# Kernel optimization log

Measured on AMD Instinct MI355X. Metric: run time of the kernel, lower is better.

The kernel has to match this reference:

```python
import jax, jax.numpy as jnp
import numpy as np

N_USERS = 100000
N_LOCAS = 50000
N = N_USERS + N_LOCAS
D = 128   # embedding_dynamic_size
K = 128   # kg entity dim
S = 128   # static dim
NK = 50000  # kg rows
E = 2048  # number of events
LN_EPS = 1e-5
NORM_EPS = 1e-12


def setup_inputs() -> dict:
    key = jax.random.key(0)
    ks = jax.random.split(key, 24)
    f = jnp.float32
    rin = D + K + 1
    s_rnn = 1.0 / np.sqrt(D)
    s_pred = 1.0 / np.sqrt(2 * S + 2 * D + K)
    inp = {
        'embedding': jax.random.normal(ks[0], (N, D), f),
        'static': jax.random.normal(ks[1], (N, S), f),
        'kg': jax.random.normal(ks[2], (NK, K), f),
        'W_ih_u': jax.random.normal(ks[3], (D, rin), f) * s_rnn,
        'b_ih_u': jax.random.normal(ks[4], (D,), f) * s_rnn,
        'W_hh_u': jax.random.normal(ks[5], (D, D), f) * s_rnn,
        'b_hh_u': jax.random.normal(ks[6], (D,), f) * s_rnn,
        'W_ih_l': jax.random.normal(ks[7], (D, rin), f) * s_rnn,
        'b_ih_l': jax.random.normal(ks[8], (D,), f) * s_rnn,
        'W_hh_l': jax.random.normal(ks[9], (D, D), f) * s_rnn,
        'b_hh_l': jax.random.normal(ks[10], (D,), f) * s_rnn,
        'w_proj': jax.random.normal(ks[11], (D,), f),   # NormalLinear(1, D) weight, std=1/sqrt(1)=1
        'b_proj': jax.random.normal(ks[12], (D,), f),
        'ln_g': jnp.ones((D + K,), f),
        'ln_b': jnp.zeros((D + K,), f),
        'W_pred': jax.random.normal(ks[13], (S + D, 2 * S + 2 * D + K), f) * s_pred,
        'b_pred': jnp.zeros((S + D,), f),
        'delta_u': jax.random.uniform(ks[14], (E,), f),
        'delta_l': jax.random.uniform(ks[15], (E,), f),
        'idx_user': jax.random.randint(ks[16], (E,), 0, N_USERS, jnp.int32),
        'idx_loca': jax.random.randint(ks[17], (E,), 0, N_LOCAS, jnp.int32),
        'idx_prev': jax.random.randint(ks[18], (E,), 0, N_LOCAS, jnp.int32),
        'idx_know': jax.random.randint(ks[19], (E,), 0, NK, jnp.int32),
        'num_users': N_USERS,
    }
    return inp


def reference(embedding, static, kg, W_ih_u, b_ih_u, W_hh_u, b_hh_u,
              W_ih_l, b_ih_l, W_hh_l, b_hh_l, w_proj, b_proj, ln_g, ln_b,
              W_pred, b_pred, delta_u, delta_l,
              idx_user, idx_loca, idx_prev, idx_know, num_users):
    sg = jax.lax.stop_gradient

    def l2n(x):  # F.normalize along the feature dim (row vector)
        return x / jnp.maximum(jnp.linalg.norm(x), NORM_EPS)

    # event index preprocessing (matches idx_loca + num_users etc.)
    xs = (idx_user, idx_loca + num_users, idx_prev + num_users, idx_know,
          delta_u, delta_l)

    def step(carry, ev):
        emb, loss = carry
        iu, il, ip, ik, du, dl = ev
        u = emb[iu]        # [D]
        l = emb[il]        # [D]
        p = emb[ip]        # [D]
        kgr = kg[ik]       # [K]
        # projection: u * (1 + Linear(1->D)(delta_u))
        proj = u * (1.0 + w_proj * du + b_proj)
        # layer_norm over concat([emb_prev, kg_row]) of size D+K
        x = jnp.concatenate([p, kgr])
        mu = x.mean()
        var = jnp.mean((x - mu) ** 2)
        ln = (x - mu) / jnp.sqrt(var + LN_EPS) * ln_g + ln_b
        meta = jnp.concatenate([proj, ln, static[ip], static[iu]])  # [2S+2D+K]
        pred = W_pred @ meta + b_pred                               # [S+D]
        tgt = jnp.concatenate([l, static[il]])
        loss_pred = jnp.mean((pred - sg(tgt)) ** 2)
        # RNNCell updates (tanh), then L2-normalize
        x_u = jnp.concatenate([l, kgr, du[None]])
        new_u = l2n(jnp.tanh(W_ih_u @ x_u + b_ih_u + W_hh_u @ u + b_hh_u))
        x_l = jnp.concatenate([u, kgr, dl[None]])
        new_l = l2n(jnp.tanh(W_ih_l @ x_l + b_ih_l + W_hh_l @ l + b_hh_l))
        loss = loss + loss_pred \
                    + jnp.mean((new_u - sg(u)) ** 2) \
                    + jnp.mean((new_l - sg(l)) ** 2)
        emb = emb.at[iu].set(new_u).at[il].set(new_l)
        return (emb, loss), None

    (emb, loss), _ = jax.lax.scan(
        step, (embedding, jnp.asarray(0.0, embedding.dtype)), xs)
    return emb, loss
```

## Files before the change

### kernel.cpp

```cpp
#include <hip/hip_runtime.h>

#define DEVINL static __device__ __forceinline__

typedef float f32x4 __attribute__((ext_vector_type(4)));

constexpr int NUSER = 100000;
constexpr int D     = 128;
constexpr int METAN = 640;
constexpr int NT    = 256;
constexpr int CH    = 4;
constexpr int KP4   = 160;
constexpr int KR4   = 96;
constexpr int NCPY  = 1024;
constexpr int STW   = 640;

struct Params {
  const float *emb_in, *stat, *kg;
  const float *Wihu, *bihu, *Whhu, *bhhu;
  const float *Wihl, *bihl, *Whhl, *bhhl;
  const float *wproj, *bproj, *lng, *lnb, *Wpred, *bpred;
  const float *deltau, *deltal;
  const int *idxu, *idxl, *idxp, *idxk;
  float *emb;
  float *loss_slot;
  float *WpredT;
  float *WrnnT;
  float *brnn;
  float *wcol;
  float *loss_ev;
  float *stash;
  int *cnt_u, *cnt_w, *cnt_t;
  int *flag_u, *flag_l;
  int *done;
  int E, N, NLOC, NWORK;
};

DEVINL float loadx(const float* p) {
  return __hip_atomic_load(p, __ATOMIC_RELAXED, __HIP_MEMORY_SCOPE_AGENT);
}
DEVINL void storex(float* p, float v) {
  __hip_atomic_store(p, v, __ATOMIC_RELAXED, __HIP_MEMORY_SCOPE_AGENT);
}
DEVINL int loadcnt(const int* p) {
  return __hip_atomic_load(p, __ATOMIC_RELAXED, __HIP_MEMORY_SCOPE_AGENT);
}
DEVINL void storei(int* p, int v) {
  __hip_atomic_store(p, v, __ATOMIC_RELAXED, __HIP_MEMORY_SCOPE_AGENT);
}
DEVINL void sigadd(int* pp) {
  __hip_atomic_fetch_add(pp, 1, __ATOMIC_RELAXED, __HIP_MEMORY_SCOPE_AGENT);
}
DEVINL float dot4(float4 a, float4 b) { return a.x*b.x + a.y*b.y + a.z*b.z + a.w*b.w; }

DEVINL float4 block_sum4(float4 v, float4* s4) {
  #pragma unroll
  for (int o = 32; o; o >>= 1) {
    v.x += __shfl_xor(v.x, o, 64); v.y += __shfl_xor(v.y, o, 64);
    v.z += __shfl_xor(v.z, o, 64); v.w += __shfl_xor(v.w, o, 64);
  }
  if ((threadIdx.x & 63) == 0) s4[threadIdx.x >> 6] = v;
  __syncthreads();
  float4 r;
  r.x = s4[0].x + s4[1].x + s4[2].x + s4[3].x;
  r.y = s4[0].y + s4[1].y + s4[2].y + s4[3].y;
  r.z = s4[0].z + s4[1].z + s4[2].z + s4[3].z;
  r.w = s4[0].w + s4[1].w + s4[2].w + s4[3].w;
  __syncthreads();
  return r;
}

DEVINL void half_sum4(float4 v, float4* s4, float4* lo, float4* hi) {
  #pragma unroll
  for (int o = 32; o; o >>= 1) {
    v.x += __shfl_xor(v.x, o, 64); v.y += __shfl_xor(v.y, o, 64);
    v.z += __shfl_xor(v.z, o, 64); v.w += __shfl_xor(v.w, o, 64);
  }
  if ((threadIdx.x & 63) == 0) s4[threadIdx.x >> 6] = v;
  __syncthreads();
  lo->x = s4[0].x + s4[1].x; lo->y = s4[0].y + s4[1].y;
  lo->z = s4[0].z + s4[1].z; lo->w = s4[0].w + s4[1].w;
  hi->x = s4[2].x + s4[3].x; hi->y = s4[2].y + s4[3].y;
  hi->z = s4[2].z + s4[3].z; hi->w = s4[2].w + s4[3].w;
  __syncthreads();
}

__global__ void k_init(Params p) {
  int tid = blockIdx.x * NT + threadIdx.x;
  int stride = gridDim.x * NT;
  for (int e = tid; e < p.E; e += stride) {
    p.flag_u[p.idxu[e]] = 1;
    p.flag_l[p.idxl[e]] = 1;
  }
  for (int idx = tid; idx < 256 * KP4; idx += stride) {
    int j = idx / KP4, k4 = idx - j * KP4;
    float4 v = *(const float4*)(p.Wpred + (size_t)j * METAN + k4 * 4);
    ((float4*)p.WpredT)[k4 * 256 + j] = v;
  }
  for (int idx = tid; idx < 256 * KR4; idx += stride) {
    int j = idx / KR4, k4 = idx - j * KR4;
    int i = j & 127;
    const float* Wih = (j < 128) ? p.Wihu : p.Wihl;
    const float* Whh = (j < 128) ? p.Whhu : p.Whhl;
    float4 v; float* vp = (float*)&v;
    #pragma unroll
    for (int e = 0; e < 4; ++e) {
      int k = k4 * 4 + e;
      vp[e] = (k < 256) ? Wih[(size_t)i * 257 + k] : Whh[(size_t)i * 128 + (k - 256)];
    }
    ((float4*)p.WrnnT)[k4 * 256 + j] = v;
  }
  for (int j = tid; j < 256; j += stride) {
    int i = j & 127;
    p.brnn[j] = (j < 128) ? p.bihu[i] + p.bhhu[i] : p.bihl[i] + p.bhhl[i];
    p.wcol[j] = (j < 128) ? p.Wihu[(size_t)i * 257 + 256] : p.Wihl[(size_t)i * 257 + 256];
  }
}

__global__ __launch_bounds__(NT, 2) void k_main(Params p) {
  __shared__ __align__(16) float s_meta[CH][METAN];
  __shared__ __align__(16) float s_u[CH][D], s_l[CH][D], s_p[CH][D], s_kg[CH][D], s_sil[CH][D];
  __shared__ float4 s_r4[4];
  __shared__ unsigned long long s_redu[4][CH];
  __shared__ int s_ev[8][CH];
  __shared__ float s_dd[2][CH];

  const int tid = threadIdx.x, w = tid >> 6, lane = tid & 63;
  const int bid = blockIdx.x;

  if (bid >= p.NWORK && bid < p.NWORK + NCPY) {
    size_t gid = (size_t)(bid - p.NWORK) * NT + tid;
    size_t gs  = (size_t)NCPY * NT;
    size_t n4  = (size_t)p.N * 32;
    const f32x4* src = (const f32x4*)p.emb_in;
    f32x4* dst = (f32x4*)p.emb;
    size_t g = gid;
    for (; g + 3 * gs < n4; g += 4 * gs) {
      size_t g0 = g, g1 = g + gs, g2 = g + 2 * gs, g3 = g + 3 * gs;
      int r0 = (int)(g0 >> 5), r1 = (int)(g1 >> 5), r2 = (int)(g2 >> 5), r3 = (int)(g3 >> 5);
      int f0 = (r0 < NUSER) ? p.flag_u[r0] : p.flag_l[r0 - NUSER];
      int f1 = (r1 < NUSER) ? p.flag_u[r1] : p.flag_l[r1 - NUSER];
      int f2 = (r2 < NUSER) ? p.flag_u[r2] : p.flag_l[r2 - NUSER];
      int f3 = (r3 < NUSER) ? p.flag_u[r3] : p.flag_l[r3 - NUSER];
      f32x4 v0 = src[g0], v1 = src[g1], v2 = src[g2], v3 = src[g3];
      if (!f0) dst[g0] = v0;
      if (!f1) dst[g1] = v1;
      if (!f2) dst[g2] = v2;
      if (!f3) dst[g3] = v3;
    }
    for (; g < n4; g += gs) {
      int r = (int)(g >> 5);
      int f = (r < NUSER) ? p.flag_u[r] : p.flag_l[r - NUSER];
      f32x4 v = src[g];
      if (!f) dst[g] = v;
    }
    return;
  }

  const bool is_chain = (bid < p.NWORK);
  const int c = is_chain ? bid : bid - p.NWORK - NCPY;
  const int base = c * CH;
  const int nev = min(CH, p.E - base);
  if (nev <= 0) return;

  int iu_[CH], il_[CH], ip_[CH], ik_[CH];
  #pragma unroll
  for (int e = 0; e < CH; ++e) {
    int t = base + e; bool v = e < nev;
    iu_[e] = v ? p.idxu[t] : -1;
    il_[e] = v ? p.idxl[t] : -1;
    ip_[e] = v ? p.idxp[t] : -1;
    ik_[e] = v ? p.idxk[t] : 0;
  }

  if (is_chain) {
    float du_[CH], dl_[CH];
    #pragma unroll
    for (int e = 0; e < CH; ++e) {
      int t = base + e; bool v = e < nev;
      du_[e] = v ? p.deltau[t] : 0.f;
      dl_[e] = v ? p.deltal[t] : 0.f;
    }

    unsigned long long pk[CH] = {0ull,0ull,0ull,0ull};
    for (int s = tid; s < base; s += NT) {
      int ius = p.idxu[s], ils = p.idxl[s], ips = p.idxp[s];
      #pragma unroll
      for (int e = 0; e < CH; ++e) {
        unsigned long long a  = (ius == iu_[e]);
        unsigned long long wl = (ils == il_[e]);
        unsigned long long b  = (unsigned long long)((ils == il_[e]) + (ips == il_[e]));
        unsigned long long cc = (ils == ip_[e]);
        pk[e] += a | (wl << 16) | (b << 32) | (cc << 48);
      }
    }
    #pragma unroll
    for (int o = 32; o; o >>= 1) {
      #pragma unroll
      for (int e = 0; e < CH; ++e) pk[e] += __shfl_xor(pk[e], o, 64);
    }
    if (lane == 0) {
      #pragma unroll
      for (int e = 0; e < CH; ++e) s_redu[w][e] = pk[e];
    }
    __syncthreads();
    #pragma unroll
    for (int e = 0; e < CH; ++e)
      pk[e] = s_redu[0][e] + s_redu[1][e] + s_redu[2][e] + s_redu[3][e];
    __syncthreads();

    int A_[CH], WL_[CH], B_[CH], C_[CH];
    #pragma unroll
    for (int e = 0; e < CH; ++e) {
      int a  = (int)(pk[e] & 0xffff),        wl = (int)((pk[e] >> 16) & 0xffff);
      int b  = (int)((pk[e] >> 32) & 0xffff), cc = (int)((pk[e] >> 48) & 0xffff);
      #pragma unroll
      for (int s2 = 0; s2 < CH; ++s2) if (s2 < e) {
        a  += (iu_[s2] == iu_[e]);
        wl += (il_[s2] == il_[e]);
        b  += (il_[s2] == il_[e]) + (ip_[s2] == il_[e]);
        cc += (il_[s2] == ip_[e]);
      }
      A_[e] = a; WL_[e] = wl; B_[e] = b; C_[e] = cc;
    }
    bool internal = false;
    #pragma unroll
    for (int t2 = 1; t2 < CH; ++t2) if (t2 < nev) {
      #pragma unroll
      for (int s2 = 0; s2 < t2; ++s2)
        internal |= (iu_[s2] == iu_[t2]) | (il_[s2] == il_[t2]) |
                    (il_[s2] == ip_[t2]) | (ip_[s2] == il_[t2]);
    }

    if (tid == 0) {
      #pragma unroll
      for (int e = 0; e < CH; ++e) {
        s_ev[0][e] = iu_[e]; s_ev[1][e] = il_[e]; s_ev[2][e] = ip_[e];
        s_ev[3][e] = A_[e];  s_ev[4][e] = WL_[e]; s_ev[5][e] = B_[e];
        s_ev[6][e] = C_[e];  s_ev[7][e] = ik_[e];
        s_dd[0][e] = du_[e]; s_dd[1][e] = dl_[e];
      }
    }
    __syncthreads();

    auto PRELOAD = [&](int b0, int b1) {
      int e = w;
      if (e >= b0 && e < b1) {
        int iu = s_ev[0][e], ilr = s_ev[1][e] + NUSER, ipr = s_ev[2][e] + NUSER;
        int A = s_ev[3][e], WL = s_ev[4][e], Ck = s_ev[6][e], ik = s_ev[7][e];
        if (lane < 32) {
          int li = lane * 4;
          *(float4*)&s_kg[e][li] = *(const float4*)(p.kg + (size_t)ik * D + li);
        }
        int i0 = lane * 2;
        if (!A)  *(float2*)&s_u[e][i0] = *(const float2*)(p.emb_in + (size_t)iu  * D + i0);
        if (!WL) *(float2*)&s_l[e][i0] = *(const float2*)(p.emb_in + (size_t)ilr * D + i0);
        if (!Ck) *(float2*)&s_p[e][i0] = *(const float2*)(p.emb_in + (size_t)ipr * D + i0);
      }
    };

    auto SPIN = [&](int b0, int b1) {
      if (w == 0) {
        int e = b0 + lane;
        bool act = lane < (b1 - b0);
        int iu = 0, il = 0, ip = 0, A = 0, Bc = 0, Cc = 0;
        if (act) {
          iu = s_ev[0][e]; il = s_ev[1][e]; ip = s_ev[2][e];
          A = s_ev[3][e]; Bc = s_ev[5][e]; Cc = s_ev[6][e];
        }
        int guard = 0;
        while (true) {
          int x = loadcnt(&p.cnt_u[iu]);
          int y = loadcnt(&p.cnt_t[il]);
          int z = loadcnt(&p.cnt_w[ip]);
          bool ok = (!act) | ((x >= A) & (y >= Bc) & (z >= Cc));
          if (__all(ok)) break;
          if (++guard > (1 << 22)) break;
          __builtin_amdgcn_s_sleep(1);
        }
      }
      __syncthreads();
    };

    auto POSTLOAD = [&](int b0, int b1) {
      int e = w;
      if (e >= b0 && e < b1) {
        int iu = s_ev[0][e], ilr = s_ev[1][e] + NUSER, ipr = s_ev[2][e] + NUSER;
        int A = s_ev[3][e], WL = s_ev[4][e], Ck = s_ev[6][e];
        int i0 = lane * 2;
        if (A) {
          s_u[e][i0]   = loadx(p.emb + (size_t)iu * D + i0);
          s_u[e][i0+1] = loadx(p.emb + (size_t)iu * D + i0 + 1);
        }
        if (WL) {
          s_l[e][i0]   = loadx(p.emb + (size_t)ilr * D + i0);
          s_l[e][i0+1] = loadx(p.emb + (size_t)ilr * D + i0 + 1);
        }
        if (Ck) {
          s_p[e][i0]   = loadx(p.emb + (size_t)ipr * D + i0);
          s_p[e][i0+1] = loadx(p.emb + (size_t)ipr * D + i0 + 1);
        }
      }
    };

    auto RNNPROC = [&](int b0, int b1) {
      __syncthreads();
      const bool uc = (tid < 128);
      const float4* xo0 = (const float4*)(uc ? s_l[0] : s_u[0]);
      const float4* xo1 = (const float4*)(uc ? s_l[1] : s_u[1]);
      const float4* xo2 = (const float4*)(uc ? s_l[2] : s_u[2]);
      const float4* xo3 = (const float4*)(uc ? s_l[3] : s_u[3]);
      const float4* xk0 = (const float4*)s_kg[0];
      const float4* xk1 = (const float4*)s_kg[1];
      const float4* xk2 = (const float4*)s_kg[2];
      const float4* xk3 = (const float4*)s_kg[3];
      const float4* xs0 = (const float4*)(uc ? s_u[0] : s_l[0]);
      const float4* xs1 = (const float4*)(uc ? s_u[1] : s_l[1]);
      const float4* xs2 = (const float4*)(uc ? s_u[2] : s_l[2]);
      const float4* xs3 = (const float4*)(uc ? s_u[3] : s_l[3]);
      float ra0 = 0.f, ra1 = 0.f, ra2 = 0.f, ra3 = 0.f;
      const float4* wr = (const float4*)p.WrnnT + tid;
      #pragma unroll 8
      for (int k4 = 0; k4 < 32; ++k4) {
        float4 wv = wr[k4 * 256];
        ra0 += dot4(wv, xo0[k4]); ra1 += dot4(wv, xo1[k4]);
        ra2 += dot4(wv, xo2[k4]); ra3 += dot4(wv, xo3[k4]);
      }
      #pragma unroll 8
      for (int k4 = 32; k4 < 64; ++k4) {
        float4 wv = wr[k4 * 256];
        ra0 += dot4(wv, xk0[k4-32]); ra1 += dot4(wv, xk1[k4-32]);
        ra2 += dot4(wv, xk2[k4-32]); ra3 += dot4(wv, xk3[k4-32]);
      }
      #pragma unroll 8
      for (int k4 = 64; k4 < 96; ++k4) {
        float4 wv = wr[k4 * 256];
        ra0 += dot4(wv, xs0[k4-64]); ra1 += dot4(wv, xs1[k4-64]);
        ra2 += dot4(wv, xs2[k4-64]); ra3 += dot4(wv, xs3[k4-64]);
      }
      float brn = p.brnn[tid], wcv = p.wcol[tid];
      float d0 = uc ? s_dd[0][0] : s_dd[1][0];
      float d1 = uc ? s_dd[0][1] : s_dd[1][1];
      float d2 = uc ? s_dd[0][2] : s_dd[1][2];
      float d3 = uc ? s_dd[0][3] : s_dd[1][3];
      float h0 = tanhf(ra0 + brn + wcv * d0), h1 = tanhf(ra1 + brn + wcv * d1);
      float h2v = tanhf(ra2 + brn + wcv * d2), h3 = tanhf(ra3 + brn + wcv * d3);

      float4 SU, SL;
      half_sum4(make_float4(h0*h0, h1*h1, h2v*h2v, h3*h3), s_r4, &SU, &SL);
      float s0 = uc ? SU.x : SL.x, s1 = uc ? SU.y : SL.y;
      float s2 = uc ? SU.z : SL.z, s3 = uc ? SU.w : SL.w;
      float n0 = h0 / fmaxf(sqrtf(s0), 1e-12f), n1 = h1 / fmaxf(sqrtf(s1), 1e-12f);
      float n2 = h2v / fmaxf(sqrtf(s2), 1e-12f), n3 = h3 / fmaxf(sqrtf(s3), 1e-12f);

      float nv[CH] = {n0, n1, n2, n3};
      #pragma unroll
      for (int e = 0; e < CH; ++e) if (e >= b0 && e < b1) {
        if (tid < 128) storex(p.emb + (size_t)s_ev[0][e] * D + tid, nv[e]);
        else           storex(p.emb + ((size_t)s_ev[1][e] + NUSER) * D + (tid - 128), nv[e]);
      }
      __syncthreads();

      if (tid >= b0 && tid < b1) {
        __builtin_amdgcn_fence(__ATOMIC_RELEASE, "agent");
        sigadd(&p.cnt_u[s_ev[0][tid]]);
        sigadd(&p.cnt_t[s_ev[1][tid]]);
        sigadd(&p.cnt_w[s_ev[1][tid]]);
        sigadd(&p.cnt_t[s_ev[2][tid]]);
      }

      #pragma unroll
      for (int e = 0; e < CH; ++e) if (e >= b0 && e < b1) {
        float* st = p.stash + (size_t)(base + e) * STW;
        if (tid < 128) {
          storex(st + tid,       s_u[e][tid]);
          storex(st + 256 + tid, s_p[e][tid]);
          storex(st + 384 + tid, nv[e]);
        } else {
          int i = tid - 128;
          storex(st + 128 + i, s_l[e][i]);
          storex(st + 512 + i, nv[e]);
        }
      }
    };

    if (!internal) {
      PRELOAD(0, nev);
      SPIN(0, nev);
      POSTLOAD(0, nev);
      RNNPROC(0, nev);
    } else {
      for (int e = 0; e < nev; ++e) {
        PRELOAD(e, e + 1);
        SPIN(e, e + 1);
        POSTLOAD(e, e + 1);
        RNNPROC(e, e + 1);
      }
    }
    __syncthreads();
    if (tid == 0) storei(&p.done[c], 1);
    return;
  }

  {
    if (w == 0) {
      int guard = 0;
      while (!loadcnt(&p.done[c])) {
        if (++guard > (1 << 22)) break;
        __builtin_amdgcn_s_sleep(1);
      }
    }
    __syncthreads();

    if (w < nev) {
      int e = w;
      const float* st = p.stash + (size_t)(base + e) * STW;
      int iu = iu_[e], ilr = il_[e] + NUSER, ipr = ip_[e] + NUSER, ik = ik_[e];
      int i0 = lane * 2;
      s_u[e][i0]   = loadx(st + i0);
      s_u[e][i0+1] = loadx(st + i0 + 1);
      s_l[e][i0]   = loadx(st + 128 + i0);
      s_l[e][i0+1] = loadx(st + 128 + i0 + 1);
      s_p[e][i0]   = loadx(st + 256 + i0);
      s_p[e][i0+1] = loadx(st + 256 + i0 + 1);
      int h2 = lane >> 5, li = (lane & 31) * 4;
      if (h2 == 0) {
        *(float4*)&s_kg[e][li]         = *(const float4*)(p.kg   + (size_t)ik  * D + li);
        *(float4*)&s_meta[e][512 + li] = *(const float4*)(p.stat + (size_t)iu  * D + li);
      } else {
        *(float4*)&s_meta[e][384 + li] = *(const float4*)(p.stat + (size_t)ipr * D + li);
        *(float4*)&s_sil[e][li]        = *(const float4*)(p.stat + (size_t)ilr * D + li);
      }
    }
    __syncthreads();

    if (w < nev) {
      int e = w;
      float du = p.deltau[base + e];
      float4 xv = (lane < 32) ? *(const float4*)&s_p[e][lane * 4]
                              : *(const float4*)&s_kg[e][(lane - 32) * 4];
      float sm = xv.x + xv.y + xv.z + xv.w;
      #pragma unroll
      for (int o = 32; o; o >>= 1) sm += __shfl_xor(sm, o, 64);
      float mu = sm * (1.f / 256.f);
      float4 d = make_float4(xv.x - mu, xv.y - mu, xv.z - mu, xv.w - mu);
      float vs = d.x*d.x + d.y*d.y + d.z*d.z + d.w*d.w;
      #pragma unroll
      for (int o = 32; o; o >>= 1) vs += __shfl_xor(vs, o, 64);
      float rstd = rsqrtf(vs * (1.f / 256.f) + 1e-5f);
      int idx2 = lane * 4;
      float4 g  = *(const float4*)&p.lng[idx2];
      float4 bb = *(const float4*)&p.lnb[idx2];
      float4 lnv = make_float4(d.x*rstd*g.x + bb.x, d.y*rstd*g.y + bb.y,
                               d.z*rstd*g.z + bb.z, d.w*rstd*g.w + bb.w);
      if (lane < 32) *(float4*)&s_meta[e][128 + idx2] = lnv;
      else           *(float4*)&s_meta[e][128 + idx2] = lnv;
      int i0 = lane * 2;
      #pragma unroll
      for (int j = 0; j < 2; ++j) {
        int i = i0 + j;
        s_meta[e][i] = s_u[e][i] * (1.f + p.wproj[i] * du + p.bproj[i]);
      }
    }
    __syncthreads();

    const bool uc = (tid < 128);
    const float4* m40 = (const float4*)&s_meta[0][0];
    const float4* m41 = (const float4*)&s_meta[1][0];
    const float4* m42 = (const float4*)&s_meta[2][0];
    const float4* m43 = (const float4*)&s_meta[3][0];
    float pa0 = 0.f, pa1 = 0.f, pa2 = 0.f, pa3 = 0.f;
    const float4* wp = (const float4*)p.WpredT + tid;
    #pragma unroll 8
    for (int k4 = 0; k4 < KP4; ++k4) {
      float4 wv = wp[k4 * 256];
      pa0 += dot4(wv, m40[k4]); pa1 += dot4(wv, m41[k4]);
      pa2 += dot4(wv, m42[k4]); pa3 += dot4(wv, m43[k4]);
    }
    float bp = p.bpred[tid];
    float4 ep2;
    {
      float tg0 = uc ? s_l[0][tid] : s_sil[0][tid - 128];
      float tg1 = uc ? s_l[1][tid] : s_sil[1][tid - 128];
      float tg2 = uc ? s_l[2][tid] : s_sil[2][tid - 128];
      float tg3 = uc ? s_l[3][tid] : s_sil[3][tid - 128];
      float e0 = pa0 + bp - tg0, e1 = pa1 + bp - tg1;
      float e2 = pa2 + bp - tg2, e3 = pa3 + bp - tg3;
      ep2 = make_float4(e0*e0, e1*e1, e2*e2, e3*e3);
    }
    float4 LP = block_sum4(ep2, s_r4);

    const float* st0 = p.stash + (size_t)(base + 0) * STW;
    const float* st1 = p.stash + (size_t)(base + 1) * STW;
    const float* st2 = p.stash + (size_t)(base + 2) * STW;
    const float* st3 = p.stash + (size_t)(base + 3) * STW;
    int noff = uc ? (384 + tid) : (512 + tid - 128);
    float n0 = loadx(st0 + noff), n1 = loadx(st1 + noff);
    float n2 = loadx(st2 + noff), n3 = loadx(st3 + noff);
    float o0 = uc ? s_u[0][tid] : s_l[0][tid - 128];
    float o1 = uc ? s_u[1][tid] : s_l[1][tid - 128];
    float o2 = uc ? s_u[2][tid] : s_l[2][tid - 128];
    float o3 = uc ? s_u[3][tid] : s_l[3][tid - 128];
    float q0 = n0 - o0, q1 = n1 - o1, q2 = n2 - o2, q3 = n3 - o3;
    float4 LE = block_sum4(make_float4(q0*q0, q1*q1, q2*q2, q3*q3), s_r4);

    if (tid < nev) {
      float lp = (tid == 0) ? LP.x : (tid == 1) ? LP.y : (tid == 2) ? LP.z : LP.w;
      float le = (tid == 0) ? LE.x : (tid == 1) ? LE.y : (tid == 2) ? LE.z : LE.w;
      p.loss_ev[base + tid] = lp * (1.f / 256.f) + le * (1.f / 128.f);
    }
  }
}

__global__ void k_fin(Params p) {
  __shared__ float4 s_r4[4];
  float v = 0.f;
  for (int i = threadIdx.x; i < p.E; i += NT) v += p.loss_ev[i];
  float4 r = block_sum4(make_float4(v, 0.f, 0.f, 0.f), s_r4);
  if (threadIdx.x == 0) p.loss_slot[0] = r.x;
}

extern "C" void kernel_launch(void* const* d_in, const int* in_sizes, int n_in,
                              void* d_out, int out_size, void* d_ws, size_t ws_size,
                              hipStream_t stream) {
  Params p;
  p.emb_in = (const float*)d_in[0];
  p.stat   = (const float*)d_in[1];
  p.kg     = (const float*)d_in[2];
  p.Wihu = (const float*)d_in[3];   p.bihu = (const float*)d_in[4];
  p.Whhu = (const float*)d_in[5];   p.bhhu = (const float*)d_in[6];
  p.Wihl = (const float*)d_in[7];   p.bihl = (const float*)d_in[8];
  p.Whhl = (const float*)d_in[9];   p.bhhl = (const float*)d_in[10];
  p.wproj = (const float*)d_in[11]; p.bproj = (const float*)d_in[12];
  p.lng  = (const float*)d_in[13];  p.lnb  = (const float*)d_in[14];
  p.Wpred = (const float*)d_in[15]; p.bpred = (const float*)d_in[16];
  p.deltau = (const float*)d_in[17];
  p.deltal = (const float*)d_in[18];
  p.idxu = (const int*)d_in[19];
  p.idxl = (const int*)d_in[20];
  p.idxp = (const int*)d_in[21];
  p.idxk = (const int*)d_in[22];

  p.E    = in_sizes[17];
  p.N    = in_sizes[0] / D;
  p.NLOC = p.N - NUSER;
  p.NWORK = (p.E + CH - 1) / CH;

  p.emb       = (float*)d_out;
  p.loss_slot = (float*)d_out + (size_t)p.N * D;

  char* ws = (char*)d_ws;
  size_t off = 0;
  auto take = [&](size_t bytes) {
    void* r = ws + off;
    off += (bytes + 255) & ~(size_t)255;
    return r;
  };
  p.WpredT  = (float*)take((size_t)KP4 * 256 * 16);
  p.WrnnT   = (float*)take((size_t)KR4 * 256 * 16);
  p.brnn    = (float*)take(256 * 4);
  p.wcol    = (float*)take(256 * 4);
  p.loss_ev = (float*)take((size_t)p.E * 4);
  p.stash   = (float*)take((size_t)p.E * STW * 4);
  size_t z0 = off;
  p.cnt_u   = (int*)take((size_t)NUSER * 4);
  p.cnt_w   = (int*)take((size_t)p.NLOC * 4);
  p.cnt_t   = (int*)take((size_t)p.NLOC * 4);
  p.flag_u  = (int*)take((size_t)NUSER * 4);
  p.flag_l  = (int*)take((size_t)p.NLOC * 4);
  p.done    = (int*)take((size_t)p.NWORK * 4);
  size_t zbytes = off - z0;

  hipMemsetAsync(ws + z0, 0, zbytes, stream);
  hipLaunchKernelGGL(k_init, dim3(512), dim3(NT), 0, stream, p);
  hipLaunchKernelGGL(k_main, dim3(p.NWORK * 2 + NCPY), dim3(NT), 0, stream, p);
  hipLaunchKernelGGL(k_fin,  dim3(1),   dim3(NT), 0, stream, p);
}
```

Before: 144.1 us.

## Skip dependency spin for conflict-free chunks, use nontemporal copy, deeper unroll

Adds a 'clean' fast path: when a chunk of events has no internal conflicts and no earlier writer to any of its rows, it skips the spin-wait and post-load and goes straight to the RNN step. The bulk embedding copy now uses nontemporal loads and stores to avoid polluting cache. The matvec loops are unrolled by 16 instead of 8, and stash loads for invalid events are skipped. The extra unrolling raises register pressure, and the fast path's correctness depends on the A/B/C counters fully capturing the dependencies.

```diff
diff --git a/kernel.cpp b/kernel.cpp
--- a/kernel.cpp
+++ b/kernel.cpp
@@ -141,23 +141,26 @@
       int f1 = (r1 < NUSER) ? p.flag_u[r1] : p.flag_l[r1 - NUSER];
       int f2 = (r2 < NUSER) ? p.flag_u[r2] : p.flag_l[r2 - NUSER];
       int f3 = (r3 < NUSER) ? p.flag_u[r3] : p.flag_l[r3 - NUSER];
-      f32x4 v0 = src[g0], v1 = src[g1], v2 = src[g2], v3 = src[g3];
-      if (!f0) dst[g0] = v0;
-      if (!f1) dst[g1] = v1;
-      if (!f2) dst[g2] = v2;
-      if (!f3) dst[g3] = v3;
+      f32x4 v0 = __builtin_nontemporal_load(src + g0);
+      f32x4 v1 = __builtin_nontemporal_load(src + g1);
+      f32x4 v2 = __builtin_nontemporal_load(src + g2);
+      f32x4 v3 = __builtin_nontemporal_load(src + g3);
+      if (!f0) __builtin_nontemporal_store(v0, dst + g0);
+      if (!f1) __builtin_nontemporal_store(v1, dst + g1);
+      if (!f2) __builtin_nontemporal_store(v2, dst + g2);
+      if (!f3) __builtin_nontemporal_store(v3, dst + g3);
     }
     for (; g < n4; g += gs) {
       int r = (int)(g >> 5);
       int f = (r < NUSER) ? p.flag_u[r] : p.flag_l[r - NUSER];
-      f32x4 v = src[g];
-      if (!f) dst[g] = v;
+      f32x4 v = __builtin_nontemporal_load(src + g);
+      if (!f) __builtin_nontemporal_store(v, dst + g);
     }
     return;
   }
 
-  const bool is_chain = (bid < p.NWORK);
-  const int c = is_chain ? bid : bid - p.NWORK - NCPY;
+  const bool is_worker = (bid < p.NWORK);
+  const int c = is_worker ? bid : bid - p.NWORK - NCPY;
   const int base = c * CH;
   const int nev = min(CH, p.E - base);
   if (nev <= 0) return;
@@ -172,7 +175,7 @@
     ik_[e] = v ? p.idxk[t] : 0;
   }
 
-  if (is_chain) {
+  if (is_worker) {
     float du_[CH], dl_[CH];
     #pragma unroll
     for (int e = 0; e < CH; ++e) {
@@ -230,6 +233,10 @@
         internal |= (iu_[s2] == iu_[t2]) | (il_[s2] == il_[t2]) |
                     (il_[s2] == ip_[t2]) | (ip_[s2] == il_[t2]);
     }
+    bool clean = !internal;
+    #pragma unroll
+    for (int e = 0; e < CH; ++e) if (e < nev)
+      clean = clean && (A_[e] == 0) && (B_[e] == 0) && (C_[e] == 0);
 
     if (tid == 0) {
       #pragma unroll
@@ -302,9 +309,9 @@
       }
     };
 
+    const bool uc = (tid < 128);
     auto RNNPROC = [&](int b0, int b1) {
       __syncthreads();
-      const bool uc = (tid < 128);
       const float4* xo0 = (const float4*)(uc ? s_l[0] : s_u[0]);
       const float4* xo1 = (const float4*)(uc ? s_l[1] : s_u[1]);
       const float4* xo2 = (const float4*)(uc ? s_l[2] : s_u[2]);
@@ -319,19 +326,19 @@
       const float4* xs3 = (const float4*)(uc ? s_u[3] : s_l[3]);
       float ra0 = 0.f, ra1 = 0.f, ra2 = 0.f, ra3 = 0.f;
       const float4* wr = (const float4*)p.WrnnT + tid;
-      #pragma unroll 8
+      #pragma unroll 16
       for (int k4 = 0; k4 < 32; ++k4) {
         float4 wv = wr[k4 * 256];
         ra0 += dot4(wv, xo0[k4]); ra1 += dot4(wv, xo1[k4]);
         ra2 += dot4(wv, xo2[k4]); ra3 += dot4(wv, xo3[k4]);
       }
-      #pragma unroll 8
+      #pragma unroll 16
       for (int k4 = 32; k4 < 64; ++k4) {
         float4 wv = wr[k4 * 256];
         ra0 += dot4(wv, xk0[k4-32]); ra1 += dot4(wv, xk1[k4-32]);
         ra2 += dot4(wv, xk2[k4-32]); ra3 += dot4(wv, xk3[k4-32]);
       }
-      #pragma unroll 8
+      #pragma unroll 16
       for (int k4 = 64; k4 < 96; ++k4) {
         float4 wv = wr[k4 * 256];
         ra0 += dot4(wv, xs0[k4-64]); ra1 += dot4(wv, xs1[k4-64]);
@@ -383,13 +390,17 @@
       }
     };
 
-    if (!internal) {
+    if (clean) {
+      PRELOAD(0, nev);
+      RNNPROC(0, nev);
+    } else if (!internal) {
       PRELOAD(0, nev);
       SPIN(0, nev);
       POSTLOAD(0, nev);
       RNNPROC(0, nev);
     } else {
-      for (int e = 0; e < nev; ++e) {
+      #pragma unroll
+      for (int e = 0; e < CH; ++e) if (e < nev) {
         PRELOAD(e, e + 1);
         SPIN(e, e + 1);
         POSTLOAD(e, e + 1);
@@ -413,8 +424,9 @@
 
     if (w < nev) {
       int e = w;
-      const float* st = p.stash + (size_t)(base + e) * STW;
+      int t = base + e;
       int iu = iu_[e], ilr = il_[e] + NUSER, ipr = ip_[e] + NUSER, ik = ik_[e];
+      const float* st = p.stash + (size_t)t * STW;
       int i0 = lane * 2;
       s_u[e][i0]   = loadx(st + i0);
       s_u[e][i0+1] = loadx(st + i0 + 1);
@@ -450,10 +462,9 @@
       int idx2 = lane * 4;
       float4 g  = *(const float4*)&p.lng[idx2];
       float4 bb = *(const float4*)&p.lnb[idx2];
-      float4 lnv = make_float4(d.x*rstd*g.x + bb.x, d.y*rstd*g.y + bb.y,
-                               d.z*rstd*g.z + bb.z, d.w*rstd*g.w + bb.w);
-      if (lane < 32) *(float4*)&s_meta[e][128 + idx2] = lnv;
-      else           *(float4*)&s_meta[e][128 + idx2] = lnv;
+      *(float4*)&s_meta[e][128 + idx2] = make_float4(
+        d.x*rstd*g.x + bb.x, d.y*rstd*g.y + bb.y,
+        d.z*rstd*g.z + bb.z, d.w*rstd*g.w + bb.w);
       int i0 = lane * 2;
       #pragma unroll
       for (int j = 0; j < 2; ++j) {
@@ -470,7 +481,7 @@
     const float4* m43 = (const float4*)&s_meta[3][0];
     float pa0 = 0.f, pa1 = 0.f, pa2 = 0.f, pa3 = 0.f;
     const float4* wp = (const float4*)p.WpredT + tid;
-    #pragma unroll 8
+    #pragma unroll 16
     for (int k4 = 0; k4 < KP4; ++k4) {
       float4 wv = wp[k4 * 256];
       pa0 += dot4(wv, m40[k4]); pa1 += dot4(wv, m41[k4]);
@@ -494,8 +505,8 @@
     const float* st2 = p.stash + (size_t)(base + 2) * STW;
     const float* st3 = p.stash + (size_t)(base + 3) * STW;
     int noff = uc ? (384 + tid) : (512 + tid - 128);
-    float n0 = loadx(st0 + noff), n1 = loadx(st1 + noff);
-    float n2 = loadx(st2 + noff), n3 = loadx(st3 + noff);
+    float n0 = loadx(st0 + noff), n1 = (nev > 1) ? loadx(st1 + noff) : 0.f;
+    float n2 = (nev > 2) ? loadx(st2 + noff) : 0.f, n3 = (nev > 3) ? loadx(st3 + noff) : 0.f;
     float o0 = uc ? s_u[0][tid] : s_l[0][tid - 128];
     float o1 = uc ? s_u[1][tid] : s_l[1][tid - 128];
     float o2 = uc ? s_u[2][tid] : s_l[2][tid - 128];
@@ -571,7 +582,7 @@
   size_t zbytes = off - z0;
 
   hipMemsetAsync(ws + z0, 0, zbytes, stream);
-  hipLaunchKernelGGL(k_init, dim3(512), dim3(NT), 0, stream, p);
+  hipLaunchKernelGGL(k_init, dim3(512),                dim3(NT), 0, stream, p);
   hipLaunchKernelGGL(k_main, dim3(p.NWORK * 2 + NCPY), dim3(NT), 0, stream, p);
-  hipLaunchKernelGGL(k_fin,  dim3(1),   dim3(NT), 0, stream, p);
-}
+  hipLaunchKernelGGL(k_fin,  dim3(1),                  dim3(NT), 0, stream, p);
+}
```

After: 192.0 us. +33.2%, slower.
